# Optimization experiments

Hardware: AMD Instinct MI355X
Metric: run time of the kernel (lower is better)

The kernel has to match this reference:

```python
import jax, jax.numpy as jnp
import numpy as np

B, S, E = 2, 2048, 1024
H, D = 16, 64          # num_heads, head_dim
FF = 4096              # ff_dim = 4*E
EPS = 1e-5


def _layer_norm(x, g, b):
    mu = jnp.mean(x, axis=-1, keepdims=True)
    var = jnp.mean(jnp.square(x - mu), axis=-1, keepdims=True)
    return (x - mu) * jax.lax.rsqrt(var + EPS) * g + b


def setup_inputs() -> dict:
    key = jax.random.key(0)
    ks = jax.random.split(key, 9)
    s = lambda fan_in: 1.0 / np.sqrt(fan_in)
    return {
        "x": jax.random.normal(ks[0], (B, S, E), dtype=jnp.float32),
        "w_qkv": jax.random.uniform(ks[1], (3 * E, E), jnp.float32, -s(E), s(E)),
        "b_qkv": jnp.zeros((3 * E,), jnp.float32),
        "w_out": jax.random.uniform(ks[2], (E, E), jnp.float32, -s(E), s(E)),
        "b_out": jnp.zeros((E,), jnp.float32),
        "g1": jnp.ones((E,), jnp.float32),
        "beta1": jnp.zeros((E,), jnp.float32),
        "w_fc1": jax.random.uniform(ks[3], (FF, E), jnp.float32, -s(E), s(E)),
        "b_fc1": jnp.zeros((FF,), jnp.float32),
        "w_fc2": jax.random.uniform(ks[4], (E, FF), jnp.float32, -s(FF), s(FF)),
        "b_fc2": jnp.zeros((E,), jnp.float32),
        "g2": jnp.ones((E,), jnp.float32),
        "beta2": jnp.zeros((E,), jnp.float32),
    }


def reference(x, w_qkv, b_qkv, w_out, b_out, g1, beta1, w_fc1, b_fc1, w_fc2, b_fc2, g2, beta2):
    scale = 1.0 / np.sqrt(D)
    # QKV projection: [B,S,3E] -> [3,B,H,S,D]
    qkv = (x @ w_qkv.T + b_qkv).reshape(B, S, 3, H, D).transpose(2, 0, 3, 1, 4)
    q, k, v = qkv[0], qkv[1], qkv[2]
    attn = jax.nn.softmax(jnp.einsum('bhqd,bhkd->bhqk', q, k) * scale, axis=-1)
    out = jnp.einsum('bhqk,bhkd->bhqd', attn, v)          # [B,H,S,D]
    out = out.transpose(0, 2, 1, 3).reshape(B, S, E)
    attn_out = out @ w_out.T + b_out
    x1 = _layer_norm(x + attn_out, g1, beta1)
    h = jax.nn.gelu(x1 @ w_fc1.T + b_fc1, approximate=False)  # torch GELU = exact erf
    ff_out = h @ w_fc2.T + b_fc2
    return _layer_norm(x1 + ff_out, g2, beta2)
```

## Files before the change

kernel.cpp:

```cpp
#include <hip/hip_runtime.h>
#include <hip/hip_bf16.h>
#include <math.h>
#include <type_traits>

typedef __hip_bfloat16 bf16;
using short8  = __attribute__((ext_vector_type(8))) short;
using short4v = __attribute__((ext_vector_type(4))) short;
using f32x4   = __attribute__((ext_vector_type(4))) float;

#define TS 2048
#define TH 16
#define TD 64
#define TE 1024
#define T2E 2048

__device__ __forceinline__ void gload16(void* lds, const void* g) {
    __builtin_amdgcn_global_load_lds(
        (__attribute__((address_space(1))) void*)g,
        (__attribute__((address_space(3))) void*)lds, 16, 0, 0);
}

__device__ __forceinline__ uint32_t pktrunc(float a, float b) {
    return (__builtin_bit_cast(uint32_t, a) >> 16) |
           (__builtin_bit_cast(uint32_t, b) & 0xFFFF0000u);
}

__global__ __launch_bounds__(256) void f2b_multi(
    const float* __restrict__ s0, bf16* __restrict__ d0,
    const float* __restrict__ s1, bf16* __restrict__ d1,
    const float* __restrict__ s2, bf16* __restrict__ d2,
    const float* __restrict__ s3, bf16* __restrict__ d3,
    const float* __restrict__ s4, bf16* __restrict__ d4)
{
    int blk = blockIdx.x;
    const float* s; bf16* d; int base;
    if (blk < 2048)      { s = s0; d = d0; base = 0; }
    else if (blk < 3584) { s = s1; d = d1; base = 2048; }
    else if (blk < 4096) { s = s2; d = d2; base = 3584; }
    else if (blk < 6144) { s = s3; d = d3; base = 4096; }
    else                 { s = s4; d = d4; base = 6144; }
    size_t i = ((size_t)(blk - base) * 256 + threadIdx.x) * 8;
    float4 a = *(const float4*)&s[i];
    float4 b = *(const float4*)&s[i + 4];
    bf16 t[8];
    t[0] = __float2bfloat16(a.x); t[1] = __float2bfloat16(a.y);
    t[2] = __float2bfloat16(a.z); t[3] = __float2bfloat16(a.w);
    t[4] = __float2bfloat16(b.x); t[5] = __float2bfloat16(b.y);
    t[6] = __float2bfloat16(b.z); t[7] = __float2bfloat16(b.w);
    *(uint4*)&d[i] = *(uint4*)t;
}

template <typename TC, bool GELU, bool QS, bool WVT, int BN>
__global__ __launch_bounds__(512, 2) void gemm256(
    const bf16* __restrict__ A, const bf16* __restrict__ Bw,
    const float* __restrict__ bias, TC* __restrict__ C,
    bf16* __restrict__ vTout, int M, int N, int K, int kLen, int Cstride)
{
    constexpr int NB = BN / 64;
    constexpr int NI = BN / 64;
    constexpr int WN = BN / 4;
    __shared__ bf16 As[2][256 * 64];
    __shared__ bf16 Bs[2][BN * 64];

    const int t    = threadIdx.x;
    const int lane = t & 63;
    const int wv   = t >> 6;
    const int wr   = wv >> 2;
    const int wc   = wv & 3;
    const int lr   = lane & 15;
    const int lq   = lane >> 4;

    const int gx  = gridDim.x, gxy = gridDim.x * gridDim.y;
    const int nwg = gxy * gridDim.z;
    const int id  = blockIdx.x + gx * blockIdx.y + gxy * blockIdx.z;
    const int sid = (id & 7) * (nwg >> 3) + (id >> 3);
    const int zIdx  = sid / gxy;
    const int rem   = sid - zIdx * gxy;
    const int tm    = rem / gx;
    const int mBase = tm * 256;
    const int nBase = (rem - tm * gx) * BN;
    const int kOff  = zIdx * kLen;

    const int sr = t >> 3;
    const int sc = (((t & 7) ^ ((t >> 3) & 7)) * 8);
    const int NT = kLen >> 6;

    const bf16* aPt = A  + (size_t)(mBase + sr) * K + sc;
    const bf16* bPt = Bw + (size_t)(nBase + sr) * K + sc;

    f32x4 acc[8][NI];
    #pragma unroll
    for (int mi = 0; mi < 8; mi++)
        #pragma unroll
        for (int ni = 0; ni < NI; ni++)
            acc[mi][ni] = (f32x4){0.f, 0.f, 0.f, 0.f};

    auto stage = [&](int b, int k0) {
        #pragma unroll
        for (int i = 0; i < 4; i++)
            gload16(&As[b][i * 4096 + wv * 512],
                    aPt + (size_t)(i * 64) * K + k0);
        #pragma unroll
        for (int i = 0; i < NB; i++)
            gload16(&Bs[b][i * 4096 + wv * 512],
                    bPt + (size_t)(i * 64) * K + k0);
    };

    stage(0, kOff);
    for (int kt = 0; kt < NT; ++kt) {
        const int cur = kt & 1;
        if (kt + 1 < NT) {
            stage(cur ^ 1, kOff + (kt + 1) * 64);
            if constexpr (BN == 256)
                asm volatile("s_waitcnt vmcnt(8)" ::: "memory");
            else if constexpr (BN == 192)
                asm volatile("s_waitcnt vmcnt(7)" ::: "memory");
            else
                asm volatile("s_waitcnt vmcnt(6)" ::: "memory");
        } else {
            asm volatile("s_waitcnt vmcnt(0)" ::: "memory");
        }
        __builtin_amdgcn_s_barrier();
        asm volatile("" ::: "memory");

        short8 bfr[NI][2];
        #pragma unroll
        for (int ni = 0; ni < NI; ni++)
            #pragma unroll
            for (int ks = 0; ks < 2; ks++) {
                int row = wc * WN + ni * 16 + lr;
                int col = (ks * 32 + lq * 8) ^ ((lr & 7) * 8);
                bfr[ni][ks] = *(const short8*)&Bs[cur][row * 64 + col];
            }
        #pragma unroll
        for (int mi = 0; mi < 8; mi++) {
            int row = wr * 128 + mi * 16 + lr;
            int c0 = (lq * 8) ^ ((lr & 7) * 8);
            int c1 = (32 + lq * 8) ^ ((lr & 7) * 8);
            short8 a0 = *(const short8*)&As[cur][row * 64 + c0];
            short8 a1 = *(const short8*)&As[cur][row * 64 + c1];
            #pragma unroll
            for (int ni = 0; ni < NI; ni++) {
                acc[mi][ni] = __builtin_amdgcn_mfma_f32_16x16x32_bf16(
                    a0, bfr[ni][0], acc[mi][ni], 0, 0, 0);
                acc[mi][ni] = __builtin_amdgcn_mfma_f32_16x16x32_bf16(
                    a1, bfr[ni][1], acc[mi][ni], 0, 0, 0);
            }
        }
        asm volatile("s_waitcnt lgkmcnt(0)" ::: "memory");
        __builtin_amdgcn_s_barrier();
    }

    const size_t cOff = (size_t)zIdx * M * Cstride;
    #pragma unroll
    for (int mi = 0; mi < 8; mi++) {
        #pragma unroll
        for (int ni = 0; ni < NI; ni++) {
            int cc = nBase + wc * WN + ni * 16 + lr;
            float bv = (zIdx == 0) ? bias[cc] : 0.f;
            int r0 = mBase + wr * 128 + mi * 16 + lq * 4;
            bool vpath = false;
            if constexpr (WVT) {
                if (cc >= 2 * TE) {
                    vpath = true;
                    int d  = cc - 2 * TE;
                    int s0 = r0 & (TS - 1);
                    int bb = r0 >> 11;
                    int pos = (s0 & ~31) | (((s0 >> 2) & 3) << 3)
                            | (((s0 >> 4) & 1) << 2);
                    bf16 ob[4];
                    #pragma unroll
                    for (int i = 0; i < 4; i++)
                        ob[i] = __float2bfloat16(acc[mi][ni][i] + bv);
                    *(uint2*)&vTout[((size_t)(bb * TH + (d >> 6)) * TD + (d & 63))
                                    * TS + pos] = *(uint2*)ob;
                }
            }
            if (!vpath) {
                #pragma unroll
                for (int i = 0; i < 4; i++) {
                    float v = acc[mi][ni][i] + bv;
                    if constexpr (GELU)
                        v = 0.5f * v * (1.0f + erff(v * 0.70710678118f));
                    if constexpr (QS)
                        if (cc < TE) v *= 0.180336880111f;
                    if constexpr (std::is_same_v<TC, bf16>)
                        C[cOff + (size_t)(r0 + i) * Cstride + cc] = __float2bfloat16(v);
                    else
                        C[cOff + (size_t)(r0 + i) * Cstride + cc] = v;
                }
            }
        }
    }
}

__global__ __launch_bounds__(256, 4) void attn_flash(
    const bf16* __restrict__ qkv, const bf16* __restrict__ vT,
    bf16* __restrict__ attnO)
{
    __shared__ bf16 Ks[128 * 72];
    __shared__ bf16 Vt[64 * 136];

    const int t    = threadIdx.x;
    const int lane = t & 63;
    const int wv   = t >> 6;
    const int c    = lane & 15;
    const int u    = lane >> 4;
    const int bid  = blockIdx.x;
    const int bh   = (bid & 7) * 4 + ((bid >> 3) & 3);
    const int qt   = bid >> 5;
    const int h = bh & 15, b = bh >> 4;
    const size_t tokBase = (size_t)b * TS;
    const int qrow = qt * 64 + wv * 16 + c;

    short8 qf[2];
    #pragma unroll
    for (int kc = 0; kc < 2; kc++)
        qf[kc] = *(const short8*)&qkv[(tokBase + qrow) * T2E + h * TD + kc * 32 + u * 8];

    f32x4 oacc[4];
    #pragma unroll
    for (int di = 0; di < 4; di++) oacc[di] = (f32x4){0.f, 0.f, 0.f, 0.f};
    float lsum = 0.f;

    const int vd = t >> 2;
    const int vc = (t & 3) * 8;
    const bf16* vbase = &vT[((size_t)bh * TD + vd) * TS + vc];

    for (int it = 0; it < 16; it++) {
        const int kb0 = it * 128;
        __syncthreads();

        #pragma unroll
        for (int i = 0; i < 4; i++) {
            int l = t + i * 256;
            int r = l >> 3, ch = (l & 7) * 8;
            *(uint4*)&Ks[r * 72 + ch] =
                *(const uint4*)&qkv[(tokBase + kb0 + r) * T2E + TE + h * TD + ch];
        }
        #pragma unroll
        for (int i = 0; i < 4; i++)
            *(uint4*)&Vt[vd * 136 + vc + i * 32] = *(const uint4*)&vbase[kb0 + i * 32];
        __syncthreads();

        f32x4 sacc[8];
        #pragma unroll
        for (int kc = 0; kc < 2; kc++) {
            #pragma unroll
            for (int kb = 0; kb < 8; kb++) {
                short8 kf = *(const short8*)&Ks[(kb * 16 + c) * 72 + kc * 32 + u * 8];
                sacc[kb] = __builtin_amdgcn_mfma_f32_16x16x32_bf16(
                    kf, qf[kc],
                    kc == 0 ? (f32x4){0.f, 0.f, 0.f, 0.f} : sacc[kb], 0, 0, 0);
            }
        }

        #pragma unroll
        for (int p = 0; p < 4; p++) {
            union { uint32_t d[2]; short4v s; } pb0, pb1;
            {
                float a0 = exp2f(sacc[2*p][0]);
                float a1 = exp2f(sacc[2*p][1]);
                float a2 = exp2f(sacc[2*p][2]);
                float a3 = exp2f(sacc[2*p][3]);
                float b0 = exp2f(sacc[2*p+1][0]);
                float b1 = exp2f(sacc[2*p+1][1]);
                float b2 = exp2f(sacc[2*p+1][2]);
                float b3 = exp2f(sacc[2*p+1][3]);
                lsum += (a0 + a1) + (a2 + a3) + (b0 + b1) + (b2 + b3);
                pb0.d[0] = pktrunc(a0, a1); pb0.d[1] = pktrunc(a2, a3);
                pb1.d[0] = pktrunc(b0, b1); pb1.d[1] = pktrunc(b2, b3);
            }
            #pragma unroll
            for (int di = 0; di < 4; di++) {
                short8 vv = *(const short8*)&Vt[(di * 16 + c) * 136 + p * 32 + u * 8];
                short4v lo = __builtin_shufflevector(vv, vv, 0, 1, 2, 3);
                short4v hi = __builtin_shufflevector(vv, vv, 4, 5, 6, 7);
                oacc[di] = __builtin_amdgcn_mfma_f32_16x16x16bf16_1k(
                    lo, pb0.s, oacc[di], 0, 0, 0);
                oacc[di] = __builtin_amdgcn_mfma_f32_16x16x16bf16_1k(
                    hi, pb1.s, oacc[di], 0, 0, 0);
            }
        }
    }

    lsum += __shfl_xor(lsum, 16, 64);
    lsum += __shfl_xor(lsum, 32, 64);
    const float inv = 1.0f / lsum;

    #pragma unroll
    for (int di = 0; di < 4; di++) {
        bf16 ob[4];
        #pragma unroll
        for (int rg = 0; rg < 4; rg++)
            ob[rg] = __float2bfloat16(oacc[di][rg] * inv);
        *(uint2*)&attnO[(tokBase + qrow) * TE + h * TD + di * 16 + u * 4] = *(uint2*)ob;
    }
}

__global__ __launch_bounds__(256) void add_ln3(
    const float* __restrict__ a, const float* __restrict__ p0,
    const float* __restrict__ p1, const float* __restrict__ g,
    const float* __restrict__ beta, float* __restrict__ out,
    bf16* __restrict__ outb)
{
    __shared__ float r1[256], r2[256];
    const int t = threadIdx.x;
    const size_t row = (size_t)blockIdx.x * TE;

    float4 va = *(const float4*)&a[row + t * 4];
    float4 v0 = *(const float4*)&p0[row + t * 4];
    float4 v1 = *(const float4*)&p1[row + t * 4];
    float v[4] = {va.x + v0.x + v1.x, va.y + v0.y + v1.y,
                  va.z + v0.z + v1.z, va.w + v0.w + v1.w};
    float s = 0.f, s2 = 0.f;
    #pragma unroll
    for (int i = 0; i < 4; i++) { s += v[i]; s2 += v[i] * v[i]; }
    r1[t] = s; r2[t] = s2;
    __syncthreads();
    for (int off = 128; off > 0; off >>= 1) {
        if (t < off) { r1[t] += r1[t + off]; r2[t] += r2[t + off]; }
        __syncthreads();
    }
    const float mu  = r1[0] * (1.f / 1024.f);
    const float var = r2[0] * (1.f / 1024.f) - mu * mu;
    const float rs  = rsqrtf(var + 1e-5f);
    float4 vg  = *(const float4*)&g[t * 4];
    float4 vbt = *(const float4*)&beta[t * 4];
    float o[4];
    o[0] = (v[0] - mu) * rs * vg.x + vbt.x;
    o[1] = (v[1] - mu) * rs * vg.y + vbt.y;
    o[2] = (v[2] - mu) * rs * vg.z + vbt.z;
    o[3] = (v[3] - mu) * rs * vg.w + vbt.w;
    *(float4*)&out[row + t * 4] = *(float4*)o;
    if (outb) {
        bf16 ob[4];
        #pragma unroll
        for (int i = 0; i < 4; i++) ob[i] = __float2bfloat16(o[i]);
        *(uint2*)&outb[row + t * 4] = *(uint2*)ob;
    }
}

extern "C" void kernel_launch(void* const* d_in, const int* in_sizes, int n_in,
                              void* d_out, int out_size, void* d_ws, size_t ws_size,
                              hipStream_t stream)
{
    const float* x     = (const float*)d_in[0];
    const float* w_qkv = (const float*)d_in[1];
    const float* b_qkv = (const float*)d_in[2];
    const float* w_out = (const float*)d_in[3];
    const float* b_out = (const float*)d_in[4];
    const float* g1    = (const float*)d_in[5];
    const float* beta1 = (const float*)d_in[6];
    const float* w_fc1 = (const float*)d_in[7];
    const float* b_fc1 = (const float*)d_in[8];
    const float* w_fc2 = (const float*)d_in[9];
    const float* b_fc2 = (const float*)d_in[10];
    const float* g2    = (const float*)d_in[11];
    const float* beta2 = (const float*)d_in[12];
    float* out = (float*)d_out;

    char* wsb   = (char*)d_ws;
    bf16*  qk    = (bf16*)(wsb);
    bf16*  vT    = (bf16*)(wsb + 16777216);
    bf16*  xb    = (bf16*)(wsb + 25165824);
    float* y     = (float*)(wsb);
    float* ff    = (float*)(wsb);
    bf16*  attnO = (bf16*)(wsb + 33554432);
    bf16*  x1b   = (bf16*)(wsb + 33554432);
    bf16*  wfc1b = (bf16*)(wsb + 41943040);
    bf16*  woutb = (bf16*)(wsb + 50331648);
    bf16*  wqkvb = (bf16*)(wsb + 52428800);
    float* x1    = (float*)(wsb + 67108864);
    bf16*  hbuf  = (bf16*)(wsb + 83886080);
    bf16*  wfc2b = (bf16*)(wsb + 117440512);

    const int M = 2 * TS;
    const size_t PART = (size_t)M * TE;
    dim3 blk(256), blk5(512);

    f2b_multi<<<dim3(8192), blk, 0, stream>>>(
        x, xb, w_qkv, wqkvb, w_out, woutb, w_fc1, wfc1b, w_fc2, wfc2b);

    gemm256<bf16, false, true, true, 192><<<dim3(16, 16, 1), blk5, 0, stream>>>(
        xb, wqkvb, b_qkv, qk, vT, M, 3072, TE, TE, T2E);
    attn_flash<<<dim3(1024), blk, 0, stream>>>(qk, vT, attnO);
    gemm256<float, false, false, false, 128><<<dim3(8, 16, 2), blk5, 0, stream>>>(
        attnO, woutb, b_out, y, nullptr, M, TE, TE, TE / 2, TE);
    add_ln3<<<dim3(M), blk, 0, stream>>>(x, y, y + PART, g1, beta1, x1, x1b);
    gemm256<bf16, true, false, false, 256><<<dim3(16, 16, 1), blk5, 0, stream>>>(
        x1b, wfc1b, b_fc1, hbuf, nullptr, M, 4096, TE, TE, 4096);
    gemm256<float, false, false, false, 128><<<dim3(8, 16, 2), blk5, 0, stream>>>(
        hbuf, wfc2b, b_fc2, ff, nullptr, M, TE, 4096, 2048, TE);
    add_ln3<<<dim3(M), blk, 0, stream>>>(x1, ff, ff + PART, g2, beta2, out, nullptr);
}
```

Baseline: 370.4 us.

## Add triple-buffered 128x256 split-K GEMM for out-proj and FC2

Adds a new GEMM kernel, gemm128n, with a 128x256 tile, a 3-stage LDS ring using direct global-to-LDS loads, an XOR-swizzled layout, explicit vmcnt waits and an XCD-aware block remap. It replaces the templated gemm256 for the N=1024 out-projection and FC2 GEMMs, which keep split-K=2. The goal is to hide global-load latency and give a better grid shape (256 blocks) for these narrow GEMMs. The cost is a large LDS footprint (144 KB per block) that limits occupancy to one block per CU, plus extra code to maintain.

```diff
diff --git a/kernel.cpp b/kernel.cpp
--- a/kernel.cpp
+++ b/kernel.cpp
@@ -194,6 +194,120 @@
     }
 }
 
+__global__ __launch_bounds__(512, 2) void gemm128n(
+    const bf16* __restrict__ A, const bf16* __restrict__ Bw,
+    const float* __restrict__ bias, float* __restrict__ C,
+    int M, int N, int K, int kLen)
+{
+    __shared__ bf16 As[3][128 * 64];
+    __shared__ bf16 Bs[3][256 * 64];
+
+    const int t    = threadIdx.x;
+    const int lane = t & 63;
+    const int wv   = t >> 6;
+    const int wr   = wv >> 2;
+    const int wc   = wv & 3;
+    const int lr   = lane & 15;
+    const int lq   = lane >> 4;
+
+    const int gx  = gridDim.x, gxy = gridDim.x * gridDim.y;
+    const int nwg = gxy * gridDim.z;
+    const int id  = blockIdx.x + gx * blockIdx.y + gxy * blockIdx.z;
+    const int sid = (id & 7) * (nwg >> 3) + (id >> 3);
+    const int zIdx  = sid / gxy;
+    const int rem   = sid - zIdx * gxy;
+    const int tm    = rem / gx;
+    const int mBase = tm * 128;
+    const int nBase = (rem - tm * gx) * 256;
+    const int kOff  = zIdx * kLen;
+
+    const int sr = t >> 3;
+    const int sc = (((t & 7) ^ ((t >> 3) & 7)) * 8);
+
+    const bf16* aPt = A  + (size_t)(mBase + sr) * K + sc;
+    const bf16* bPt = Bw + (size_t)(nBase + sr) * K + sc;
+
+    f32x4 acc[4][4];
+    #pragma unroll
+    for (int mi = 0; mi < 4; mi++)
+        #pragma unroll
+        for (int ni = 0; ni < 4; ni++)
+            acc[mi][ni] = (f32x4){0.f, 0.f, 0.f, 0.f};
+
+    auto stage = [&](int b, int k0) {
+        #pragma unroll
+        for (int i = 0; i < 2; i++)
+            gload16(&As[b][i * 4096 + wv * 512],
+                    aPt + (size_t)(i * 64) * K + k0);
+        #pragma unroll
+        for (int i = 0; i < 4; i++)
+            gload16(&Bs[b][i * 4096 + wv * 512],
+                    bPt + (size_t)(i * 64) * K + k0);
+    };
+
+    const int NT = kLen >> 6;
+    stage(0, kOff);
+    stage(1, kOff + 64);
+    int cur = 0;
+    for (int kt = 0; kt < NT; ++kt) {
+        if (kt + 2 < NT) {
+            int nb = cur + 2; if (nb >= 3) nb -= 3;
+            stage(nb, kOff + (kt + 2) * 64);
+            asm volatile("s_waitcnt vmcnt(12)" ::: "memory");
+        } else if (kt + 1 < NT) {
+            asm volatile("s_waitcnt vmcnt(6)" ::: "memory");
+        } else {
+            asm volatile("s_waitcnt vmcnt(0)" ::: "memory");
+        }
+        __builtin_amdgcn_s_barrier();
+        asm volatile("" ::: "memory");
+
+        short8 af[4][2], bfr[4][2];
+        #pragma unroll
+        for (int mi = 0; mi < 4; mi++)
+            #pragma unroll
+            for (int ks = 0; ks < 2; ks++) {
+                int row = wr * 64 + mi * 16 + lr;
+                int col = (ks * 32 + lq * 8) ^ ((lr & 7) * 8);
+                af[mi][ks] = *(const short8*)&As[cur][row * 64 + col];
+            }
+        #pragma unroll
+        for (int ni = 0; ni < 4; ni++)
+            #pragma unroll
+            for (int ks = 0; ks < 2; ks++) {
+                int row = wc * 64 + ni * 16 + lr;
+                int col = (ks * 32 + lq * 8) ^ ((lr & 7) * 8);
+                bfr[ni][ks] = *(const short8*)&Bs[cur][row * 64 + col];
+            }
+        #pragma unroll
+        for (int mi = 0; mi < 4; mi++)
+            #pragma unroll
+            for (int ni = 0; ni < 4; ni++) {
+                acc[mi][ni] = __builtin_amdgcn_mfma_f32_16x16x32_bf16(
+                    af[mi][0], bfr[ni][0], acc[mi][ni], 0, 0, 0);
+                acc[mi][ni] = __builtin_amdgcn_mfma_f32_16x16x32_bf16(
+                    af[mi][1], bfr[ni][1], acc[mi][ni], 0, 0, 0);
+            }
+        asm volatile("s_waitcnt lgkmcnt(0)" ::: "memory");
+        __builtin_amdgcn_s_barrier();
+        cur += 1; if (cur >= 3) cur = 0;
+    }
+
+    const size_t cOff = (size_t)zIdx * M * N;
+    #pragma unroll
+    for (int mi = 0; mi < 4; mi++) {
+        #pragma unroll
+        for (int ni = 0; ni < 4; ni++) {
+            int cc = nBase + wc * 64 + ni * 16 + lr;
+            float bv = (zIdx == 0) ? bias[cc] : 0.f;
+            int r0 = mBase + wr * 64 + mi * 16 + lq * 4;
+            #pragma unroll
+            for (int i = 0; i < 4; i++)
+                C[cOff + (size_t)(r0 + i) * N + cc] = acc[mi][ni][i] + bv;
+        }
+    }
+}
+
 __global__ __launch_bounds__(256, 4) void attn_flash(
     const bf16* __restrict__ qkv, const bf16* __restrict__ vT,
     bf16* __restrict__ attnO)
@@ -377,20 +491,20 @@
 
     const int M = 2 * TS;
     const size_t PART = (size_t)M * TE;
-    dim3 blk(256), blk5(512);
+    dim3 blk(256), blk8(512);
 
     f2b_multi<<<dim3(8192), blk, 0, stream>>>(
         x, xb, w_qkv, wqkvb, w_out, woutb, w_fc1, wfc1b, w_fc2, wfc2b);
 
-    gemm256<bf16, false, true, true, 192><<<dim3(16, 16, 1), blk5, 0, stream>>>(
+    gemm256<bf16, false, true, true, 192><<<dim3(16, 16, 1), blk8, 0, stream>>>(
         xb, wqkvb, b_qkv, qk, vT, M, 3072, TE, TE, T2E);
     attn_flash<<<dim3(1024), blk, 0, stream>>>(qk, vT, attnO);
-    gemm256<float, false, false, false, 128><<<dim3(8, 16, 2), blk5, 0, stream>>>(
-        attnO, woutb, b_out, y, nullptr, M, TE, TE, TE / 2, TE);
+    gemm128n<<<dim3(4, 32, 2), blk8, 0, stream>>>(
+        attnO, woutb, b_out, y, M, TE, TE, TE / 2);
     add_ln3<<<dim3(M), blk, 0, stream>>>(x, y, y + PART, g1, beta1, x1, x1b);
-    gemm256<bf16, true, false, false, 256><<<dim3(16, 16, 1), blk5, 0, stream>>>(
+    gemm256<bf16, true, false, false, 256><<<dim3(16, 16, 1), blk8, 0, stream>>>(
         x1b, wfc1b, b_fc1, hbuf, nullptr, M, 4096, TE, TE, 4096);
-    gemm256<float, false, false, false, 128><<<dim3(8, 16, 2), blk5, 0, stream>>>(
-        hbuf, wfc2b, b_fc2, ff, nullptr, M, TE, 4096, 2048, TE);
+    gemm128n<<<dim3(4, 32, 2), blk8, 0, stream>>>(
+        hbuf, wfc2b, b_fc2, ff, M, TE, 4096, 2048);
     add_ln3<<<dim3(M), blk, 0, stream>>>(x1, ff, ff + PART, g2, beta2, out, nullptr);
 }
```

Result: no change. 364.4 us (-1.6%).
